# Kernel tuning notes

Hardware: AMD Instinct MI355X
Metric: run time of the kernel (lower is better)

Reference implementation:

```python
import jax, jax.numpy as jnp
import numpy as np

B = 1024      # graphs per batch
N = 64        # nodes per graph
DEG = 8       # edges per node
E = B * N * DEG
V = 52737     # vocab (different_ids)
D = 512       # embed / hidden dim
K1, K2, K3 = 52, 42, 34  # ceil(0.8*64), ceil(0.8*52), ceil(0.8*42)


def setup_inputs() -> dict:
    key = jax.random.key(0)
    ks = jax.random.split(key, 40)
    x_ids = jax.random.randint(ks[0], (B * N,), 0, V)
    off = jnp.repeat(jnp.arange(B) * N, N * DEG)  # graph offsets per edge
    edge_src = jax.random.randint(ks[1], (E,), 0, N) + off
    edge_dst = jax.random.randint(ks[2], (E,), 0, N) + off

    def lin(k, i, o):
        return jax.random.normal(k, (i, o), jnp.float32) / np.float32(np.sqrt(i))

    inp = dict(x_ids=x_ids, edge_src=edge_src, edge_dst=edge_dst)
    inp['emb'] = jax.random.normal(ks[3], (V, D), jnp.float32)
    # SAGEConv params: w*l/b*l act on aggregated neighbors, w*r on root
    for i, (kl, kr) in enumerate([(4, 5), (6, 7), (8, 9)], start=1):
        inp[f'w{i}l'] = lin(ks[kl], D, D)
        inp[f'b{i}l'] = jnp.zeros((D,), jnp.float32)
        inp[f'w{i}r'] = lin(ks[kr], D, D)
    # TopKPooling score vectors
    inp['p1'] = jax.random.normal(ks[10], (D,), jnp.float32)
    inp['p2'] = jax.random.normal(ks[11], (D,), jnp.float32)
    inp['p3'] = jax.random.normal(ks[12], (D,), jnp.float32)
    dims = [(1024, 512), (512, 256), (256, 128), (128, 64), (64, 1)]
    for i, (di, do) in enumerate(dims, start=1):
        inp[f'lw{i}'] = lin(ks[12 + i], di, do)
        inp[f'lb{i}'] = jnp.zeros((do,), jnp.float32)
    return inp


def _sage(x, src, dst, emask, wl, bl, wr):
    # PyG SAGEConv: mean-aggregate neighbor messages (src -> dst), plus root term
    n = x.shape[0]
    msg = x[src] * emask[:, None]
    s = jax.ops.segment_sum(msg, dst, num_segments=n)
    c = jax.ops.segment_sum(emask, dst, num_segments=n)
    agg = s / jnp.maximum(c, 1.0)[:, None]  # empty neighborhoods -> 0
    return agg @ wl + bl + x @ wr


def _topk_pool(x, src, dst, emask, w, k):
    # PyG TopKPooling: score = tanh(x.w / ||w||); keep top-k per graph, gate x
    n = x.shape[0]
    n_per = n // B
    score = jnp.tanh((x @ w) / jnp.linalg.norm(w))
    _, idx = jax.lax.top_k(score.reshape(B, n_per), k)      # [B, k] local ids
    perm = (idx + jnp.arange(B)[:, None] * n_per).reshape(-1)  # global ids
    x_new = x[perm] * score[perm][:, None]
    new_id = jnp.full((n,), -1, jnp.int32).at[perm].set(jnp.arange(B * k, dtype=jnp.int32))
    ns, nd = new_id[src], new_id[dst]
    valid = emask * (ns >= 0) * (nd >= 0)
    ns = jnp.where(valid > 0, ns, 0)
    nd = jnp.where(valid > 0, nd, 0)
    return x_new, ns, nd, valid.astype(x.dtype)


def _readout(x, k):
    xg = x.reshape(B, k, -1)
    return jnp.concatenate([xg.max(axis=1), xg.mean(axis=1)], axis=1)  # [B, 2F]


def _forward(x_ids, edge_src, edge_dst, emb,
             w1l, b1l, w1r, w2l, b2l, w2r, w3l, b3l, w3r,
             p1, p2, p3,
             lw1, lb1, lw2, lb2, lw3, lb3, lw4, lb4, lw5, lb5):
    x = emb[x_ids]                                  # [B*N, D]
    src, dst = edge_src, edge_dst
    emask = jnp.ones((E,), x.dtype)

    x = jax.nn.relu(_sage(x, src, dst, emask, w1l, b1l, w1r))
    x, src, dst, emask = _topk_pool(x, src, dst, emask, p1, K1)
    x1 = _readout(x, K1)

    x = jax.nn.relu(_sage(x, src, dst, emask, w2l, b2l, w2r))
    x, src, dst, emask = _topk_pool(x, src, dst, emask, p2, K2)
    x2 = _readout(x, K2)

    x = jax.nn.relu(_sage(x, src, dst, emask, w3l, b3l, w3r))
    x, src, dst, emask = _topk_pool(x, src, dst, emask, p3, K3)
    x3 = _readout(x, K3)

    h = x1 + x2 + x3                                # [B, 1024]
    h = jax.nn.relu(h @ lw1 + lb1)
    h = jax.nn.relu(h @ lw2 + lb2)
    h = jax.nn.relu(h @ lw3 + lb3)
    h = jax.nn.relu(h @ lw4 + lb4)
    # dropout p=0.5 is identity in eval mode
    return jax.nn.sigmoid(h @ lw5 + lb5)[:, 0]      # [B]


def reference(x_ids, edge_src, edge_dst, emb,
              w1l, b1l, w1r, w2l, b2l, w2r, w3l, b3l, w3r,
              p1, p2, p3,
              lw1, lb1, lw2, lb2, lw3, lb3, lw4, lb4, lw5, lb5):
    return _forward(x_ids, edge_src, edge_dst, emb,
                    w1l, b1l, w1r, w2l, b2l, w2r, w3l, b3l, w3r,
                    p1, p2, p3,
                    lw1, lb1, lw2, lb2, lw3, lb3, lw4, lb4, lw5, lb5)
```

## Files before the change

kernel.cpp:

```cpp
#include <hip/hip_runtime.h>
#include <math.h>

#define BG 1024
#define EPG 512
#define ETOT (BG*EPG)
#define DIM 512
#define KP1 52
#define KP2 42
#define KP3 34
#define OFS 80

typedef unsigned int uint;
typedef short s16x8 __attribute__((ext_vector_type(8)));
typedef float f32x4 __attribute__((ext_vector_type(4)));

__device__ __forceinline__ unsigned short f2b(float x) {
    uint u = __float_as_uint(x);
    u = u + 0x7fffu + ((u >> 16) & 1u);
    return (unsigned short)(u >> 16);
}
__device__ __forceinline__ float b2f(unsigned short h) {
    return __uint_as_float(((uint)h) << 16);
}
__device__ __forceinline__ void splitf(float x, unsigned short& h, unsigned short& l) {
    h = f2b(x);
    l = f2b(x - b2f(h));
}
__device__ __forceinline__ uint pk2(unsigned short a, unsigned short b) {
    return (uint)a | ((uint)b << 16);
}

__device__ __forceinline__ void gload16(const void* g, void* l) {
    __builtin_amdgcn_global_load_lds(
        (const __attribute__((address_space(1))) void*)g,
        (__attribute__((address_space(3))) void*)l, 16, 0, 0);
}

struct WPtrs { const float* w[6]; };

__global__ void __launch_bounds__(256)
split_wT_all(WPtrs p, unsigned short* __restrict__ WT)
{
    const int wi = blockIdx.x >> 8;
    const int bb = blockIdx.x & 255;
    const float* W = p.w[wi];
    unsigned short* Thi = WT + (size_t)(2 * wi) * DIM * DIM;
    unsigned short* Tlo = Thi + (size_t)DIM * DIM;
    __shared__ float tl[32][33];
    const int t  = threadIdx.x;
    const int bx = bb & 15;
    const int by = bb >> 4;
    const int lx = t & 31, ly = t >> 5;
    for (int r = ly; r < 32; r += 8)
        tl[r][lx] = W[(size_t)(by*32 + r) * DIM + bx*32 + lx];
    __syncthreads();
    for (int r = ly; r < 32; r += 8) {
        float v = tl[lx][r];
        unsigned short h, l; splitf(v, h, l);
        size_t o = (size_t)(bx*32 + r) * DIM + by*32 + lx;
        Thi[o] = h; Tlo[o] = l;
    }
}

__global__ void __launch_bounds__(256)
sort_edges1(const int* __restrict__ esrc, const int* __restrict__ edst,
            uint* __restrict__ SE, int* __restrict__ OF)
{
    const int g = blockIdx.x;
    const int t = threadIdx.x;
    __shared__ int ld[EPG];
    __shared__ int ls[EPG];
    __shared__ int cnt4[4][64];
    __shared__ int offs[65];
    const int eb = g * EPG;
    for (int e = t; e < EPG; e += 256) {
        ld[e] = edst[eb + e] - g * 64;
        ls[e] = esrc[eb + e] - g * 64;
    }
    __syncthreads();
    {
        const int d = t & 63, q = t >> 6;
        int c = 0;
        for (int e = q * 128; e < q * 128 + 128; ++e) c += (ld[e] == d);
        cnt4[q][d] = c;
    }
    __syncthreads();
    if (t == 0) {
        int s = 0;
        for (int i = 0; i < 64; ++i) {
            offs[i] = s;
            s += cnt4[0][i] + cnt4[1][i] + cnt4[2][i] + cnt4[3][i];
        }
        offs[64] = s;
    }
    __syncthreads();
    {
        const int d = t & 63, q = t >> 6;
        int w = offs[d];
        for (int q2 = 0; q2 < q; ++q2) w += cnt4[q2][d];
        for (int e = q * 128; e < q * 128 + 128; ++e)
            if (ld[e] == d) SE[(size_t)g * EPG + (w++)] = ((uint)d << 16) | (uint)ls[e];
    }
    if (t <= 64) OF[g * OFS + t] = offs[t];
}

__global__ void __launch_bounds__(256, 4)
gather_agg(const int* __restrict__ ids, const float* __restrict__ emb,
           const uint* __restrict__ SE, const int* __restrict__ OF,
           unsigned short* __restrict__ Xhi, unsigned short* __restrict__ Xlo,
           unsigned short* __restrict__ Ghi, unsigned short* __restrict__ Glo)
{
    const int g  = blockIdx.x >> 2;
    const int c0 = (blockIdx.x & 3) * 128;
    const int t  = threadIdx.x;
    __shared__ __align__(16) float xf[64 * 128];
    __shared__ int lid[64];
    __shared__ uint el[EPG];
    __shared__ int offs[65];

    if (t < 64) lid[t] = ids[g * 64 + t];
    if (t >= 128 && t < 128 + 65) offs[t - 128] = OF[g * OFS + (t - 128)];
    __syncthreads();

    for (int s = t; s < 64 * 32; s += 256) {
        const int row = s >> 5;
        const int c4  = (s & 31) * 4;
        ((float4*)xf)[s] =
            *(const float4*)(emb + (size_t)lid[row] * DIM + c0 + c4);
    }
    const int cnt = offs[64];
    for (int e = t; e < cnt; e += 256) el[e] = SE[(size_t)g * EPG + e];
    __syncthreads();

    for (int s = t; s < 64 * 16; s += 256) {
        const int row = s >> 4;
        const int c8  = (s & 15) * 8;
        const float* src = &xf[row * 128 + c8];
        unsigned short h[8], l[8];
#pragma unroll
        for (int i = 0; i < 8; ++i) splitf(src[i], h[i], l[i]);
        uint4 Hq, Lq;
        Hq.x = pk2(h[0],h[1]); Hq.y = pk2(h[2],h[3]);
        Hq.z = pk2(h[4],h[5]); Hq.w = pk2(h[6],h[7]);
        Lq.x = pk2(l[0],l[1]); Lq.y = pk2(l[2],l[3]);
        Lq.z = pk2(l[4],l[5]); Lq.w = pk2(l[6],l[7]);
        const size_t wo = (size_t)(g * 64 + row) * DIM + c0 + c8;
        *(uint4*)(Xhi + wo) = Hq;
        *(uint4*)(Xlo + wo) = Lq;
    }

    const int ch = (t & 31) * 4;
    const int d0 = t >> 5;
    for (int d = d0; d < 64; d += 8) {
        const int cA = offs[d], cB = offs[d + 1];
        float s0 = 0.f, s1 = 0.f, s2 = 0.f, s3 = 0.f;
        for (int j = cA; j < cB; ++j) {
            const float* r = &xf[(int)(el[j] & 0xffffu) * 128 + ch];
            s0 += r[0]; s1 += r[1]; s2 += r[2]; s3 += r[3];
        }
        const float den = fmaxf((float)(cB - cA), 1.0f);
        s0 /= den; s1 /= den; s2 /= den; s3 /= den;
        unsigned short h0,h1,h2,h3,l0,l1,l2,l3;
        splitf(s0,h0,l0); splitf(s1,h1,l1); splitf(s2,h2,l2); splitf(s3,h3,l3);
        const size_t wo = (size_t)(g * 64 + d) * DIM + c0 + ch;
        *(uint2*)(Ghi + wo) = make_uint2(pk2(h0,h1), pk2(h2,h3));
        *(uint2*)(Glo + wo) = make_uint2(pk2(l0,l1), pk2(l2,l3));
    }
}

template<int NPER>
__global__ void __launch_bounds__(256, 4)
agg_sorted(const unsigned short* __restrict__ Xhi, const unsigned short* __restrict__ Xlo,
           const uint* __restrict__ SE, const int* __restrict__ OF,
           unsigned short* __restrict__ Ghi, unsigned short* __restrict__ Glo)
{
    const int g  = blockIdx.x >> 2;
    const int c0 = (blockIdx.x & 3) * 128;
    const int t  = threadIdx.x;
    __shared__ __align__(16) unsigned short xs[NPER * 256];
    __shared__ uint el[EPG];
    __shared__ int offs[NPER + 1];

    for (int s = t; s < NPER * 32; s += 256) {
        const int row  = s >> 5;
        const int half = (s >> 4) & 1;
        const int c8   = (s & 15) * 8;
        const unsigned short* src =
            (half ? Xlo : Xhi) + (size_t)(g * NPER + row) * DIM + c0 + c8;
        gload16(src, (char*)xs + (size_t)s * 16);
    }
    if (t <= NPER) offs[t] = OF[g * OFS + t];
    __syncthreads();
    const int cnt = offs[NPER];
    for (int e = t; e < cnt; e += 256) el[e] = SE[(size_t)g * EPG + e];
    __syncthreads();

    const int ch = (t & 31) * 4;
    const int d0 = t >> 5;
    for (int d = d0; d < NPER; d += 8) {
        const int cA = offs[d], cB = offs[d + 1];
        float s0 = 0.f, s1 = 0.f, s2 = 0.f, s3 = 0.f;
        for (int j = cA; j < cB; ++j) {
            const int base = (int)(el[j] & 0xffffu) * 256 + ch;
            ushort4 h = *(const ushort4*)&xs[base];
            ushort4 l = *(const ushort4*)&xs[base + 128];
            s0 += b2f(h.x) + b2f(l.x);
            s1 += b2f(h.y) + b2f(l.y);
            s2 += b2f(h.z) + b2f(l.z);
            s3 += b2f(h.w) + b2f(l.w);
        }
        const float den = fmaxf((float)(cB - cA), 1.0f);
        s0 /= den; s1 /= den; s2 /= den; s3 /= den;
        unsigned short h0,h1,h2,h3,l0,l1,l2,l3;
        splitf(s0,h0,l0); splitf(s1,h1,l1); splitf(s2,h2,l2); splitf(s3,h3,l3);
        const size_t wo = (size_t)(g * NPER + d) * DIM + c0 + ch;
        *(uint2*)(Ghi + wo) = make_uint2(pk2(h0,h1), pk2(h2,h3));
        *(uint2*)(Glo + wo) = make_uint2(pk2(l0,l1), pk2(l2,l3));
    }
}

__global__ void __launch_bounds__(256)
gemm_sage(const unsigned short* __restrict__ Ghi, const unsigned short* __restrict__ Glo,
          const unsigned short* __restrict__ WLhi, const unsigned short* __restrict__ WLlo,
          const unsigned short* __restrict__ Xhi, const unsigned short* __restrict__ Xlo,
          const unsigned short* __restrict__ WRhi, const unsigned short* __restrict__ WRlo,
          const float* __restrict__ bias, const float* __restrict__ pvec,
          float* __restrict__ C, float* __restrict__ SC4, int M)
{
    __shared__ unsigned short sA[128 * 64];
    __shared__ unsigned short sW[128 * 64];
    __shared__ float scp[128][2];

    const int t = threadIdx.x;
    const uint nwg = gridDim.x;
    const uint q8  = nwg >> 3;
    const uint bid = blockIdx.x;
    const uint sw  = (bid & 7) * q8 + (bid >> 3);
    const int  m0  = (int)(sw >> 2) * 128;
    const int  n0  = (int)(sw & 3) * 128;

    const int l  = t & 63;
    const int w  = t >> 6;
    const int wr = w >> 1;
    const int wc = w & 1;
    const int lr = l & 15;
    const int lq = l >> 4;

    f32x4 acc[4][4];
#pragma unroll
    for (int i = 0; i < 4; ++i)
#pragma unroll
        for (int j = 0; j < 4; ++j) acc[i][j] = (f32x4){0.f, 0.f, 0.f, 0.f};

    uint srow[4], soff[4];
#pragma unroll
    for (int i = 0; i < 4; ++i) {
        uint p = (uint)i * 256u + (uint)t;
        uint row = p >> 3, pc = p & 7;
        srow[i] = row;
        soff[i] = (pc ^ (row & 7u)) * 8u;
    }

#pragma unroll 1
    for (int s = 0; s < 6; ++s) {
        const int src = (s >= 3) ? 1 : 0;
        const int combo = s - src * 3;
        const unsigned short* Ap = src ? ((combo == 2) ? Xlo : Xhi)
                                       : ((combo == 2) ? Glo : Ghi);
        const unsigned short* Wp = src ? ((combo == 1) ? WRlo : WRhi)
                                       : ((combo == 1) ? WLlo : WLhi);
#pragma unroll 1
        for (int kt = 0; kt < 8; ++kt) {
            const int kb = kt * 64;
#pragma unroll
            for (int i = 0; i < 4; ++i) {
                const unsigned short* ga =
                    Ap + (size_t)(m0 + srow[i]) * DIM + kb + soff[i];
                const unsigned short* gw =
                    Wp + (size_t)(n0 + srow[i]) * DIM + kb + soff[i];
                uint p16 = ((uint)i * 256u + (uint)t) * 16u;
                gload16(ga, (char*)sA + p16);
                gload16(gw, (char*)sW + p16);
            }
            __syncthreads();
#pragma unroll
            for (int ks = 0; ks < 2; ++ks) {
                s16x8 af[4], wf[4];
#pragma unroll
                for (int i = 0; i < 4; ++i) {
                    int arow = wr * 64 + i * 16 + lr;
                    int off = arow * 128 + 16 * ((ks * 4 + lq) ^ (arow & 7));
                    af[i] = *(const s16x8*)((const char*)sA + off);
                }
#pragma unroll
                for (int j = 0; j < 4; ++j) {
                    int wrow = wc * 64 + j * 16 + lr;
                    int off = wrow * 128 + 16 * ((ks * 4 + lq) ^ (wrow & 7));
                    wf[j] = *(const s16x8*)((const char*)sW + off);
                }
#pragma unroll
                for (int i = 0; i < 4; ++i)
#pragma unroll
                    for (int j = 0; j < 4; ++j)
                        acc[i][j] = __builtin_amdgcn_mfma_f32_16x16x32_bf16(
                            af[i], wf[j], acc[i][j], 0, 0, 0);
            }
            __syncthreads();
        }
    }

    float part[4][4];
#pragma unroll
    for (int i = 0; i < 4; ++i)
#pragma unroll
        for (int r = 0; r < 4; ++r) part[i][r] = 0.f;

#pragma unroll
    for (int i = 0; i < 4; ++i) {
        const int r0 = m0 + wr * 64 + i * 16 + lq * 4;
#pragma unroll
        for (int j = 0; j < 4; ++j) {
            const int cc = n0 + wc * 64 + j * 16 + lr;
            const float bv = bias[cc];
            const float pv = pvec[cc];
#pragma unroll
            for (int r = 0; r < 4; ++r) {
                float v = fmaxf(acc[i][j][r] + bv, 0.f);
                C[(size_t)(r0 + r) * DIM + cc] = v;
                part[i][r] = fmaf(v, pv, part[i][r]);
            }
        }
    }
#pragma unroll
    for (int o = 1; o < 16; o <<= 1)
#pragma unroll
        for (int i = 0; i < 4; ++i)
#pragma unroll
            for (int r = 0; r < 4; ++r)
                part[i][r] += __shfl_xor(part[i][r], o);
    if (lr == 0) {
#pragma unroll
        for (int i = 0; i < 4; ++i)
#pragma unroll
            for (int r = 0; r < 4; ++r)
                scp[wr * 64 + i * 16 + lq * 4 + r][wc] = part[i][r];
    }
    __syncthreads();
    if (t < 128)
        SC4[(size_t)(m0 + t) * 4 + (n0 >> 7)] = scp[t][0] + scp[t][1];
}

template<int NPER, int KEEP, bool REMAP, bool INIT>
__global__ void __launch_bounds__(256)
pool_fused(const float* __restrict__ Y, const float* __restrict__ p,
           const float* __restrict__ SC4,
           unsigned short* __restrict__ Xhi, unsigned short* __restrict__ Xlo,
           const uint* __restrict__ SEp, const int* __restrict__ OFp,
           uint* __restrict__ SEn, int* __restrict__ OFn,
           float* __restrict__ H)
{
    const int g = blockIdx.x;
    const int t = threadIdx.x;
    const int wave = t >> 6, lane = t & 63;
    __shared__ float ssc[NPER];
    __shared__ float spnorm;
    __shared__ int   perm[KEEP];
    __shared__ float sgate[KEEP];
    __shared__ int   lnewid[NPER];
    __shared__ uint  eprev[EPG];
    __shared__ uint  enew[EPG];
    __shared__ int   cnt4[4][64];
    __shared__ int   offs[KEEP + 1];

    if (wave == 0) {
        float v = 0.f;
#pragma unroll
        for (int i = 0; i < 8; ++i) { float x = p[lane + i * 64]; v = fmaf(x, x, v); }
#pragma unroll
        for (int off = 32; off; off >>= 1) v += __shfl_down(v, off);
        if (lane == 0) spnorm = sqrtf(v);
    }
    __syncthreads();
    if (t < NPER) {
        const float* s4 = SC4 + (size_t)(g * NPER + t) * 4;
        float raw = s4[0] + s4[1] + s4[2] + s4[3];
        ssc[t] = tanhf(raw / spnorm);
    }
    __syncthreads();
    if (t < NPER) {
        const float s = ssc[t];
        int r = 0;
        for (int j = 0; j < NPER; ++j) {
            float sj = ssc[j];
            r += (sj > s) || (sj == s && j < t);
        }
        lnewid[t] = (r < KEEP) ? r : -1;
        if (r < KEEP) { perm[r] = t; sgate[r] = s; }
    }
    __syncthreads();

    float mx0 = -1e30f, mx1 = -1e30f, sm0 = 0.f, sm1 = 0.f;
    for (int r = 0; r < KEEP; ++r) {
        const float2 v = ((const float2*)(Y + (size_t)(g * NPER + perm[r]) * DIM))[t];
        const float sv = sgate[r];
        float a = v.x * sv, b = v.y * sv;
        mx0 = fmaxf(mx0, a); mx1 = fmaxf(mx1, b);
        sm0 += a; sm1 += b;
        unsigned short ha, la, hb, lb;
        splitf(a, ha, la); splitf(b, hb, lb);
        size_t o = (size_t)(g * KEEP + r) * DIM + 2 * t;
        *(uint*)(Xhi + o) = pk2(ha, hb);
        *(uint*)(Xlo + o) = pk2(la, lb);
    }
    {
        const size_t o = (size_t)g * 1024;
        const float me0 = sm0 / (float)KEEP, me1 = sm1 / (float)KEEP;
        if (INIT) {
            H[o + 2*t]       = mx0; H[o + 2*t + 1]       = mx1;
            H[o + 512 + 2*t] = me0; H[o + 512 + 2*t + 1] = me1;
        } else {
            H[o + 2*t]       += mx0; H[o + 2*t + 1]       += mx1;
            H[o + 512 + 2*t] += me0; H[o + 512 + 2*t + 1] += me1;
        }
    }

    if constexpr (REMAP) {
        const int cntp = OFp[g * OFS + NPER];
        for (int e = t; e < cntp; e += 256)
            eprev[e] = SEp[(size_t)g * EPG + e];
        __syncthreads();
        for (int e = t; e < cntp; e += 256) {
            const uint pk = eprev[e];
            const int ns = lnewid[pk & 0xffffu];
            const int nd = lnewid[pk >> 16];
            enew[e] = (ns >= 0 && nd >= 0)
                ? (((uint)nd << 16) | (uint)ns) : 0xFFFFFFFFu;
        }
        __syncthreads();
        {
            const int d = t & 63, q = t >> 6;
            int c = 0;
            const int e0 = q * 128;
            const int e1 = (e0 + 128 < cntp) ? e0 + 128 : cntp;
            for (int e = e0; e < e1; ++e) c += ((enew[e] >> 16) == (uint)d);
            cnt4[q][d] = c;
        }
        __syncthreads();
        if (t == 0) {
            int s = 0;
            for (int i = 0; i < KEEP; ++i) {
                offs[i] = s;
                s += cnt4[0][i] + cnt4[1][i] + cnt4[2][i] + cnt4[3][i];
            }
            offs[KEEP] = s;
        }
        __syncthreads();
        {
            const int d = t & 63, q = t >> 6;
            if (d < KEEP) {
                int w = offs[d];
                for (int q2 = 0; q2 < q; ++q2) w += cnt4[q2][d];
                const int e0 = q * 128;
                const int e1 = (e0 + 128 < cntp) ? e0 + 128 : cntp;
                for (int e = e0; e < e1; ++e)
                    if ((enew[e] >> 16) == (uint)d)
                        SEn[(size_t)g * EPG + (w++)] = enew[e];
            }
        }
        if (t <= KEEP) OFn[g * OFS + t] = offs[t];
    }
}

__global__ void __launch_bounds__(256)
mlp_fused(const float* __restrict__ H,
          const float* __restrict__ lw1, const float* __restrict__ lb1,
          const float* __restrict__ lw2, const float* __restrict__ lb2,
          const float* __restrict__ lw3, const float* __restrict__ lb3,
          const float* __restrict__ lw4, const float* __restrict__ lb4,
          const float* __restrict__ lw5, const float* __restrict__ lb5,
          float* __restrict__ out)
{
    __shared__ float h0[2][1024];
    __shared__ float y1[2][512];
    __shared__ float y2[2][256];
    __shared__ float y3[2][128];
    __shared__ float y4[2][64];
    const int t = threadIdx.x;
    const int r0 = blockIdx.x * 2;

    {
        float4 a = *(const float4*)&H[(size_t)r0 * 1024 + t * 4];
        float4 b = *(const float4*)&H[(size_t)(r0 + 1) * 1024 + t * 4];
        *(float4*)&h0[0][t * 4] = a;
        *(float4*)&h0[1][t * 4] = b;
    }
    __syncthreads();
    {
        float a00 = 0.f, a01 = 0.f, a10 = 0.f, a11 = 0.f;
        const int c = t * 2;
#pragma unroll 4
        for (int k = 0; k < 1024; ++k) {
            float2 wv = *(const float2*)&lw1[(size_t)k * 512 + c];
            float x0 = h0[0][k], x1 = h0[1][k];
            a00 = fmaf(x0, wv.x, a00); a01 = fmaf(x0, wv.y, a01);
            a10 = fmaf(x1, wv.x, a10); a11 = fmaf(x1, wv.y, a11);
        }
        y1[0][c]     = fmaxf(a00 + lb1[c], 0.f);
        y1[0][c + 1] = fmaxf(a01 + lb1[c + 1], 0.f);
        y1[1][c]     = fmaxf(a10 + lb1[c], 0.f);
        y1[1][c + 1] = fmaxf(a11 + lb1[c + 1], 0.f);
    }
    __syncthreads();
    {
        float a0 = 0.f, a1 = 0.f;
#pragma unroll 4
        for (int k = 0; k < 512; ++k) {
            float wv = lw2[(size_t)k * 256 + t];
            a0 = fmaf(y1[0][k], wv, a0);
            a1 = fmaf(y1[1][k], wv, a1);
        }
        y2[0][t] = fmaxf(a0 + lb2[t], 0.f);
        y2[1][t] = fmaxf(a1 + lb2[t], 0.f);
    }
    __syncthreads();
    if (t < 128) {
        float a0 = 0.f, a1 = 0.f;
#pragma unroll 4
        for (int k = 0; k < 256; ++k) {
            float wv = lw3[(size_t)k * 128 + t];
            a0 = fmaf(y2[0][k], wv, a0);
            a1 = fmaf(y2[1][k], wv, a1);
        }
        y3[0][t] = fmaxf(a0 + lb3[t], 0.f);
        y3[1][t] = fmaxf(a1 + lb3[t], 0.f);
    }
    __syncthreads();
    if (t < 64) {
        float a0 = 0.f, a1 = 0.f;
#pragma unroll 4
        for (int k = 0; k < 128; ++k) {
            float wv = lw4[(size_t)k * 64 + t];
            a0 = fmaf(y3[0][k], wv, a0);
            a1 = fmaf(y3[1][k], wv, a1);
        }
        y4[0][t] = fmaxf(a0 + lb4[t], 0.f);
        y4[1][t] = fmaxf(a1 + lb4[t], 0.f);
    }
    __syncthreads();
    const int wv = t >> 6, ln = t & 63;
    if (wv < 2) {
        float v = y4[wv][ln] * lw5[ln];
#pragma unroll
        for (int off = 32; off; off >>= 1) v += __shfl_down(v, off);
        if (ln == 0) out[r0 + wv] = 1.f / (1.f + expf(-(v + lb5[0])));
    }
}

extern "C" void kernel_launch(void* const* d_in, const int* in_sizes, int n_in,
                              void* d_out, int out_size, void* d_ws, size_t ws_size,
                              hipStream_t stream)
{
    const int*   x_ids = (const int*)d_in[0];
    const int*   esrc  = (const int*)d_in[1];
    const int*   edst  = (const int*)d_in[2];
    const float* emb   = (const float*)d_in[3];
    const float* w1l = (const float*)d_in[4],  *b1l = (const float*)d_in[5],  *w1r = (const float*)d_in[6];
    const float* w2l = (const float*)d_in[7],  *b2l = (const float*)d_in[8],  *w2r = (const float*)d_in[9];
    const float* w3l = (const float*)d_in[10], *b3l = (const float*)d_in[11], *w3r = (const float*)d_in[12];
    const float* p1  = (const float*)d_in[13];
    const float* p2  = (const float*)d_in[14];
    const float* p3  = (const float*)d_in[15];
    const float* lw1 = (const float*)d_in[16], *lb1 = (const float*)d_in[17];
    const float* lw2 = (const float*)d_in[18], *lb2 = (const float*)d_in[19];
    const float* lw3 = (const float*)d_in[20], *lb3 = (const float*)d_in[21];
    const float* lw4 = (const float*)d_in[22], *lb4 = (const float*)d_in[23];
    const float* lw5 = (const float*)d_in[24], *lb5 = (const float*)d_in[25];
    float* out = (float*)d_out;

    const size_t PL = (size_t)65536 * DIM;
    unsigned short* Xhi = (unsigned short*)d_ws;
    unsigned short* Xlo = Xhi + PL;
    unsigned short* Ghi = Xlo + PL;
    unsigned short* Glo = Ghi + PL;
    float* Cc  = (float*)(Glo + PL);
    float* H   = Cc + PL;
    float* SC4 = H + (size_t)1024 * 1024;
    uint*  SE1 = (uint*)(SC4 + (size_t)65536 * 4);
    uint*  SE2 = SE1 + ETOT;
    uint*  SE3 = SE2 + ETOT;
    int*   OF1 = (int*)(SE3 + ETOT);
    int*   OF2 = OF1 + BG * OFS;
    int*   OF3 = OF2 + BG * OFS;
    unsigned short* WT = (unsigned short*)(OF3 + BG * OFS);
    const size_t WSZ = (size_t)DIM * DIM;
    unsigned short *w1lh = WT + 0*WSZ,  *w1ll = WT + 1*WSZ;
    unsigned short *w1rh = WT + 2*WSZ,  *w1rl = WT + 3*WSZ;
    unsigned short *w2lh = WT + 4*WSZ,  *w2ll = WT + 5*WSZ;
    unsigned short *w2rh = WT + 6*WSZ,  *w2rl = WT + 7*WSZ;
    unsigned short *w3lh = WT + 8*WSZ,  *w3ll = WT + 9*WSZ;
    unsigned short *w3rh = WT + 10*WSZ, *w3rl = WT + 11*WSZ;

    WPtrs wp;
    wp.w[0] = w1l; wp.w[1] = w1r; wp.w[2] = w2l;
    wp.w[3] = w2r; wp.w[4] = w3l; wp.w[5] = w3r;
    split_wT_all<<<6 * 256, 256, 0, stream>>>(wp, WT);

    sort_edges1<<<BG, 256, 0, stream>>>(esrc, edst, SE1, OF1);
    gather_agg<<<BG * 4, 256, 0, stream>>>(x_ids, emb, SE1, OF1,
                                           Xhi, Xlo, Ghi, Glo);
    gemm_sage<<<(65536/128)*4, 256, 0, stream>>>(Ghi, Glo, w1lh, w1ll,
                                                 Xhi, Xlo, w1rh, w1rl,
                                                 b1l, p1, Cc, SC4, 65536);
    pool_fused<64, KP1, true, true><<<BG, 256, 0, stream>>>(
        Cc, p1, SC4, Xhi, Xlo, SE1, OF1, SE2, OF2, H);

    agg_sorted<KP1><<<BG * 4, 256, 0, stream>>>(Xhi, Xlo, SE2, OF2, Ghi, Glo);
    gemm_sage<<<(53248/128)*4, 256, 0, stream>>>(Ghi, Glo, w2lh, w2ll,
                                                 Xhi, Xlo, w2rh, w2rl,
                                                 b2l, p2, Cc, SC4, 53248);
    pool_fused<KP1, KP2, true, false><<<BG, 256, 0, stream>>>(
        Cc, p2, SC4, Xhi, Xlo, SE2, OF2, SE3, OF3, H);

    agg_sorted<KP2><<<BG * 4, 256, 0, stream>>>(Xhi, Xlo, SE3, OF3, Ghi, Glo);
    gemm_sage<<<(43008/128)*4, 256, 0, stream>>>(Ghi, Glo, w3lh, w3ll,
                                                 Xhi, Xlo, w3rh, w3rl,
                                                 b3l, p3, Cc, SC4, 43008);
    pool_fused<KP2, KP3, false, false><<<BG, 256, 0, stream>>>(
        Cc, p3, SC4, Xhi, Xlo, nullptr, nullptr, nullptr, nullptr, H);

    mlp_fused<<<512, 256, 0, stream>>>(H, lw1, lb1, lw2, lb2, lw3, lb3,
                                       lw4, lb4, lw5, lb5, out);
}
```

Measured before the change: 1.152 ms.

## Fuse top-k pooling with neighbor aggregation into one column-sliced kernel

Merges pool_fused and agg_sorted into pool_agg, launched with four blocks per graph, each handling a 128-column slice. Each block keeps its gated fp32 slice in shared memory and aggregates neighbor means from it directly, so the next layer's features are not re-read from global memory and two kernel launches disappear. Each slice block now repeats the score, top-k and edge remap work (four times the redundant sort), and uses more shared memory. The final pool skips writing X because nothing consumes it.

Measured after the change: 1.214 ms. 1.05x slower.

```diff
diff --git a/kernel.cpp b/kernel.cpp
--- a/kernel.cpp
+++ b/kernel.cpp
@@ -168,57 +168,6 @@
     }
 }
 
-template<int NPER>
-__global__ void __launch_bounds__(256, 4)
-agg_sorted(const unsigned short* __restrict__ Xhi, const unsigned short* __restrict__ Xlo,
-           const uint* __restrict__ SE, const int* __restrict__ OF,
-           unsigned short* __restrict__ Ghi, unsigned short* __restrict__ Glo)
-{
-    const int g  = blockIdx.x >> 2;
-    const int c0 = (blockIdx.x & 3) * 128;
-    const int t  = threadIdx.x;
-    __shared__ __align__(16) unsigned short xs[NPER * 256];
-    __shared__ uint el[EPG];
-    __shared__ int offs[NPER + 1];
-
-    for (int s = t; s < NPER * 32; s += 256) {
-        const int row  = s >> 5;
-        const int half = (s >> 4) & 1;
-        const int c8   = (s & 15) * 8;
-        const unsigned short* src =
-            (half ? Xlo : Xhi) + (size_t)(g * NPER + row) * DIM + c0 + c8;
-        gload16(src, (char*)xs + (size_t)s * 16);
-    }
-    if (t <= NPER) offs[t] = OF[g * OFS + t];
-    __syncthreads();
-    const int cnt = offs[NPER];
-    for (int e = t; e < cnt; e += 256) el[e] = SE[(size_t)g * EPG + e];
-    __syncthreads();
-
-    const int ch = (t & 31) * 4;
-    const int d0 = t >> 5;
-    for (int d = d0; d < NPER; d += 8) {
-        const int cA = offs[d], cB = offs[d + 1];
-        float s0 = 0.f, s1 = 0.f, s2 = 0.f, s3 = 0.f;
-        for (int j = cA; j < cB; ++j) {
-            const int base = (int)(el[j] & 0xffffu) * 256 + ch;
-            ushort4 h = *(const ushort4*)&xs[base];
-            ushort4 l = *(const ushort4*)&xs[base + 128];
-            s0 += b2f(h.x) + b2f(l.x);
-            s1 += b2f(h.y) + b2f(l.y);
-            s2 += b2f(h.z) + b2f(l.z);
-            s3 += b2f(h.w) + b2f(l.w);
-        }
-        const float den = fmaxf((float)(cB - cA), 1.0f);
-        s0 /= den; s1 /= den; s2 /= den; s3 /= den;
-        unsigned short h0,h1,h2,h3,l0,l1,l2,l3;
-        splitf(s0,h0,l0); splitf(s1,h1,l1); splitf(s2,h2,l2); splitf(s3,h3,l3);
-        const size_t wo = (size_t)(g * NPER + d) * DIM + c0 + ch;
-        *(uint2*)(Ghi + wo) = make_uint2(pk2(h0,h1), pk2(h2,h3));
-        *(uint2*)(Glo + wo) = make_uint2(pk2(l0,l1), pk2(l2,l3));
-    }
-}
-
 __global__ void __launch_bounds__(256)
 gemm_sage(const unsigned short* __restrict__ Ghi, const unsigned short* __restrict__ Glo,
           const unsigned short* __restrict__ WLhi, const unsigned short* __restrict__ WLlo,
@@ -350,27 +299,27 @@
         SC4[(size_t)(m0 + t) * 4 + (n0 >> 7)] = scp[t][0] + scp[t][1];
 }
 
-template<int NPER, int KEEP, bool REMAP, bool INIT>
-__global__ void __launch_bounds__(256)
-pool_fused(const float* __restrict__ Y, const float* __restrict__ p,
-           const float* __restrict__ SC4,
-           unsigned short* __restrict__ Xhi, unsigned short* __restrict__ Xlo,
-           const uint* __restrict__ SEp, const int* __restrict__ OFp,
-           uint* __restrict__ SEn, int* __restrict__ OFn,
-           float* __restrict__ H)
+template<int NPER, int KEEP, bool REMAP, bool INIT, bool WRITEX>
+__global__ void __launch_bounds__(256, 4)
+pool_agg(const float* __restrict__ Y, const float* __restrict__ p,
+         const float* __restrict__ SC4,
+         unsigned short* __restrict__ Xhi, unsigned short* __restrict__ Xlo,
+         const uint* __restrict__ SEp, const int* __restrict__ OFp,
+         uint* __restrict__ SEn, int* __restrict__ OFn,
+         unsigned short* __restrict__ Ghi, unsigned short* __restrict__ Glo,
+         float* __restrict__ H)
 {
-    const int g = blockIdx.x;
-    const int t = threadIdx.x;
+    const int g  = blockIdx.x >> 2;
+    const int sl = blockIdx.x & 3;
+    const int c0 = sl * 128;
+    const int t  = threadIdx.x;
     const int wave = t >> 6, lane = t & 63;
+    __shared__ __align__(16) float xf[KEEP * 128];
     __shared__ float ssc[NPER];
     __shared__ float spnorm;
     __shared__ int   perm[KEEP];
     __shared__ float sgate[KEEP];
     __shared__ int   lnewid[NPER];
-    __shared__ uint  eprev[EPG];
-    __shared__ uint  enew[EPG];
-    __shared__ int   cnt4[4][64];
-    __shared__ int   offs[KEEP + 1];
 
     if (wave == 0) {
         float v = 0.f;
@@ -383,8 +332,7 @@
     __syncthreads();
     if (t < NPER) {
         const float* s4 = SC4 + (size_t)(g * NPER + t) * 4;
-        float raw = s4[0] + s4[1] + s4[2] + s4[3];
-        ssc[t] = tanhf(raw / spnorm);
+        ssc[t] = tanhf((s4[0] + s4[1] + s4[2] + s4[3]) / spnorm);
     }
     __syncthreads();
     if (t < NPER) {
@@ -399,33 +347,55 @@
     }
     __syncthreads();
 
-    float mx0 = -1e30f, mx1 = -1e30f, sm0 = 0.f, sm1 = 0.f;
-    for (int r = 0; r < KEEP; ++r) {
-        const float2 v = ((const float2*)(Y + (size_t)(g * NPER + perm[r]) * DIM))[t];
+    for (int s = t; s < KEEP * 32; s += 256) {
+        const int r = s >> 5, j4 = (s & 31) * 4;
+        float4 v = *(const float4*)(Y + (size_t)(g * NPER + perm[r]) * DIM + c0 + j4);
         const float sv = sgate[r];
-        float a = v.x * sv, b = v.y * sv;
-        mx0 = fmaxf(mx0, a); mx1 = fmaxf(mx1, b);
-        sm0 += a; sm1 += b;
-        unsigned short ha, la, hb, lb;
-        splitf(a, ha, la); splitf(b, hb, lb);
-        size_t o = (size_t)(g * KEEP + r) * DIM + 2 * t;
-        *(uint*)(Xhi + o) = pk2(ha, hb);
-        *(uint*)(Xlo + o) = pk2(la, lb);
-    }
-    {
-        const size_t o = (size_t)g * 1024;
-        const float me0 = sm0 / (float)KEEP, me1 = sm1 / (float)KEEP;
-        if (INIT) {
-            H[o + 2*t]       = mx0; H[o + 2*t + 1]       = mx1;
-            H[o + 512 + 2*t] = me0; H[o + 512 + 2*t + 1] = me1;
-        } else {
-            H[o + 2*t]       += mx0; H[o + 2*t + 1]       += mx1;
-            H[o + 512 + 2*t] += me0; H[o + 512 + 2*t + 1] += me1;
-        }
+        v.x *= sv; v.y *= sv; v.z *= sv; v.w *= sv;
+        *(float4*)&xf[r * 128 + j4] = v;
+    }
+    __syncthreads();
+
+    if (WRITEX) {
+        for (int s = t; s < KEEP * 16; s += 256) {
+            const int r = s >> 4, c8 = (s & 15) * 8;
+            const float* src = &xf[r * 128 + c8];
+            unsigned short h[8], l[8];
+#pragma unroll
+            for (int i = 0; i < 8; ++i) splitf(src[i], h[i], l[i]);
+            uint4 Hq, Lq;
+            Hq.x = pk2(h[0],h[1]); Hq.y = pk2(h[2],h[3]);
+            Hq.z = pk2(h[4],h[5]); Hq.w = pk2(h[6],h[7]);
+            Lq.x = pk2(l[0],l[1]); Lq.y = pk2(l[2],l[3]);
+            Lq.z = pk2(l[4],l[5]); Lq.w = pk2(l[6],l[7]);
+            const size_t wo = (size_t)(g * KEEP + r) * DIM + c0 + c8;
+            *(uint4*)(Xhi + wo) = Hq;
+            *(uint4*)(Xlo + wo) = Lq;
+        }
+    }
+    if (t < 128) {
+        float mx = -1e30f, sm = 0.f;
+        for (int r = 0; r < KEEP; ++r) {
+            float v = xf[r * 128 + t];
+            mx = fmaxf(mx, v); sm += v;
+        }
+        const size_t o = (size_t)g * 1024 + c0 + t;
+        const float me = sm / (float)KEEP;
+        if (INIT) { H[o] = mx;  H[o + 512] = me; }
+        else      { H[o] += mx; H[o + 512] += me; }
     }
 
     if constexpr (REMAP) {
-        const int cntp = OFp[g * OFS + NPER];
+        __shared__ uint  eprev[EPG];
+        __shared__ uint  enew[EPG];
+        __shared__ uint  esort[EPG];
+        __shared__ int   cnt4[4][64];
+        __shared__ int   offs[KEEP + 1];
+        __shared__ int   scnt;
+
+        if (t == 0) scnt = OFp[g * OFS + NPER];
+        __syncthreads();
+        const int cntp = scnt;
         for (int e = t; e < cntp; e += 256)
             eprev[e] = SEp[(size_t)g * EPG + e];
         __syncthreads();
@@ -463,11 +433,33 @@
                 const int e0 = q * 128;
                 const int e1 = (e0 + 128 < cntp) ? e0 + 128 : cntp;
                 for (int e = e0; e < e1; ++e)
-                    if ((enew[e] >> 16) == (uint)d)
-                        SEn[(size_t)g * EPG + (w++)] = enew[e];
+                    if ((enew[e] >> 16) == (uint)d) esort[w++] = enew[e];
             }
         }
-        if (t <= KEEP) OFn[g * OFS + t] = offs[t];
+        __syncthreads();
+        if (sl == 0) {
+            const int cntn = offs[KEEP];
+            for (int e = t; e < cntn; e += 256)
+                SEn[(size_t)g * EPG + e] = esort[e];
+            if (t <= KEEP) OFn[g * OFS + t] = offs[t];
+        }
+        const int ch = (t & 31) * 4;
+        const int d0 = t >> 5;
+        for (int d = d0; d < KEEP; d += 8) {
+            const int cA = offs[d], cB = offs[d + 1];
+            float s0 = 0.f, s1 = 0.f, s2 = 0.f, s3 = 0.f;
+            for (int j = cA; j < cB; ++j) {
+                const float* r = &xf[(int)(esort[j] & 0xffffu) * 128 + ch];
+                s0 += r[0]; s1 += r[1]; s2 += r[2]; s3 += r[3];
+            }
+            const float den = fmaxf((float)(cB - cA), 1.0f);
+            s0 /= den; s1 /= den; s2 /= den; s3 /= den;
+            unsigned short h0,h1,h2,h3,l0,l1,l2,l3;
+            splitf(s0,h0,l0); splitf(s1,h1,l1); splitf(s2,h2,l2); splitf(s3,h3,l3);
+            const size_t wo = (size_t)(g * KEEP + d) * DIM + c0 + ch;
+            *(uint2*)(Ghi + wo) = make_uint2(pk2(h0,h1), pk2(h2,h3));
+            *(uint2*)(Glo + wo) = make_uint2(pk2(l0,l1), pk2(l2,l3));
+        }
     }
 }
 
@@ -611,22 +603,21 @@
     gemm_sage<<<(65536/128)*4, 256, 0, stream>>>(Ghi, Glo, w1lh, w1ll,
                                                  Xhi, Xlo, w1rh, w1rl,
                                                  b1l, p1, Cc, SC4, 65536);
-    pool_fused<64, KP1, true, true><<<BG, 256, 0, stream>>>(
-        Cc, p1, SC4, Xhi, Xlo, SE1, OF1, SE2, OF2, H);
-
-    agg_sorted<KP1><<<BG * 4, 256, 0, stream>>>(Xhi, Xlo, SE2, OF2, Ghi, Glo);
+    pool_agg<64, KP1, true, true, true><<<BG * 4, 256, 0, stream>>>(
+        Cc, p1, SC4, Xhi, Xlo, SE1, OF1, SE2, OF2, Ghi, Glo, H);
+
     gemm_sage<<<(53248/128)*4, 256, 0, stream>>>(Ghi, Glo, w2lh, w2ll,
                                                  Xhi, Xlo, w2rh, w2rl,
                                                  b2l, p2, Cc, SC4, 53248);
-    pool_fused<KP1, KP2, true, false><<<BG, 256, 0, stream>>>(
-        Cc, p2, SC4, Xhi, Xlo, SE2, OF2, SE3, OF3, H);
-
-    agg_sorted<KP2><<<BG * 4, 256, 0, stream>>>(Xhi, Xlo, SE3, OF3, Ghi, Glo);
+    pool_agg<KP1, KP2, true, false, true><<<BG * 4, 256, 0, stream>>>(
+        Cc, p2, SC4, Xhi, Xlo, SE2, OF2, SE3, OF3, Ghi, Glo, H);
+
     gemm_sage<<<(43008/128)*4, 256, 0, stream>>>(Ghi, Glo, w3lh, w3ll,
                                                  Xhi, Xlo, w3rh, w3rl,
                                                  b3l, p3, Cc, SC4, 43008);
-    pool_fused<KP2, KP3, false, false><<<BG, 256, 0, stream>>>(
-        Cc, p3, SC4, Xhi, Xlo, nullptr, nullptr, nullptr, nullptr, H);
+    pool_agg<KP2, KP3, false, false, false><<<BG * 4, 256, 0, stream>>>(
+        Cc, p3, SC4, nullptr, nullptr, nullptr, nullptr, nullptr, nullptr,
+        nullptr, nullptr, H);
 
     mlp_fused<<<512, 256, 0, stream>>>(H, lw1, lb1, lw2, lb2, lw3, lb3,
                                        lw4, lb4, lw5, lb5, out);
```
